# Performance work log

Hardware: AMD Instinct MI355X
Metric: run time of the kernel (lower is better)

The kernel has to match this reference:

```python
import jax, jax.numpy as jnp
import numpy as np

B, N, T, W, H, ED, S, C, E = 16, 256, 64, 12, 64, 64, 5, 4, 2048
ALPHA = 1.0
FG = W + H  # gcn_in_channels = window_size + tgcn_hidden_dim


def setup_inputs() -> dict:
    key = jax.random.key(0)
    ks = jax.random.split(key, 26)
    rn = lambda k, shape: jax.random.normal(k, shape, jnp.float32) * 0.1
    x = jax.random.normal(ks[0], (B, N, T), jnp.float32)
    src = jax.random.randint(ks[1], (E,), 0, N)
    off = jax.random.randint(ks[2], (E,), 1, N)
    dst = (src + off) % N  # no self loops
    return {
        'x': x,
        'static_edge_weight': jax.random.uniform(ks[3], (E,), jnp.float32),
        'gsl_gconv_w': rn(ks[4], (FG, ED)), 'gsl_gconv_b': rn(ks[5], (ED,)),
        'gsl_w1': rn(ks[6], (ED, ED)), 'gsl_b1': rn(ks[7], (ED,)),
        'gsl_w2': rn(ks[8], (ED, ED)), 'gsl_b2': rn(ks[9], (ED,)),
        'wz_c': rn(ks[10], (1, H)), 'bz_c': rn(ks[11], (H,)),
        'wz_l': rn(ks[12], (2 * H, H)), 'bz_l': rn(ks[13], (H,)),
        'wr_c': rn(ks[14], (1, H)), 'br_c': rn(ks[15], (H,)),
        'wr_l': rn(ks[16], (2 * H, H)), 'br_l': rn(ks[17], (H,)),
        'wh_c': rn(ks[18], (1, H)), 'bh_c': rn(ks[19], (H,)),
        'wh_l': rn(ks[20], (2 * H, H)), 'bh_l': rn(ks[21], (H,)),
        'cls_w': rn(ks[22], (N * H, C)), 'cls_b': rn(ks[23], (C,)),
        'static_edge_index': jnp.stack([src, dst]).astype(jnp.int32),
    }


def _normalize(A):
    # GCN sym-norm with added self loops; A has zero diagonal by construction.
    Ahat = A + jnp.eye(N, dtype=A.dtype)
    deg = Ahat.sum(axis=-2)  # in-degree (PyG gcn_norm scatters weight on col)
    dinv = jnp.where(deg > 0, 1.0 / jnp.sqrt(deg), 0.0)
    return dinv[..., :, None] * Ahat * dinv[..., None, :]


def reference(x, static_edge_weight, gsl_gconv_w, gsl_gconv_b, gsl_w1, gsl_b1,
              gsl_w2, gsl_b2, wz_c, bz_c, wz_l, bz_l, wr_c, br_c, wr_l, br_l,
              wh_c, bh_c, wh_l, bh_l, cls_w, cls_b, static_edge_index):
    A_stat = jnp.zeros((N, N), jnp.float32).at[static_edge_index[0], static_edge_index[1]].add(static_edge_weight)
    An_stat = _normalize(A_stat)  # [N,N]

    # Sliding windows, left-padded with zeros to window_size W.
    xp = jnp.pad(x, ((0, 0), (0, 0), (W - 1, 0)))
    widx = jnp.arange(T)[:, None] + jnp.arange(W)[None, :]
    wins = jnp.transpose(xp[:, :, widx], (2, 0, 1, 3))      # [T,B,N,W]
    xts = jnp.transpose(x, (2, 0, 1))[..., None]            # [T,B,N,1]
    cnts = jnp.minimum(jnp.arange(T) + 1, S).astype(jnp.float32)
    idxs = jnp.arange(T) % S

    def gcn_s(X, Wm, b):  # static graph, out[j] = sum_i Anorm[i,j] (XW)[i]
        return jnp.einsum('ij,bif->bjf', An_stat, X @ Wm) + b

    def gcn_d(An, X, Wm, b):  # per-batch dynamic graph
        return jnp.einsum('bij,bif->bjf', An, X @ Wm) + b

    def step(carry, xs):
        h, Eh = carry
        win, xt, cnt, idx = xs
        It = jnp.concatenate([win, h], axis=-1)             # [B,N,W+H]
        df = gcn_s(It, gsl_gconv_w, gsl_gconv_b)
        de1 = jnp.tanh(ALPHA * (df @ gsl_w1 + gsl_b1))
        de2 = jnp.tanh(ALPHA * (df @ gsl_w2 + gsl_b2))
        M12 = jnp.einsum('bie,bje->bij', de1, de2)          # de1 @ de2^T
        Et = jax.nn.relu(jnp.tanh(ALPHA * (M12 - jnp.swapaxes(M12, -1, -2))))
        Eh = Eh.at[:, idx].set(Et)                          # ring buffer write
        Mt = Eh.sum(axis=1) / cnt                           # mean over filled slots
        An = _normalize(Mt)
        cz = gcn_d(An, xt, wz_c, bz_c)
        z = jax.nn.sigmoid(jnp.concatenate([cz, h], -1) @ wz_l + bz_l)
        cr = gcn_d(An, xt, wr_c, br_c)
        r = jax.nn.sigmoid(jnp.concatenate([cr, h], -1) @ wr_l + br_l)
        ch = gcn_d(An, xt, wh_c, bh_c)
        ht = jnp.tanh(jnp.concatenate([ch, h * r], -1) @ wh_l + bh_l)
        h = z * h + (1.0 - z) * ht
        return (h, Eh), None

    h0 = jnp.zeros((B, N, H), jnp.float32)
    Eh0 = jnp.zeros((B, S, N, N), jnp.float32)
    (hT, _), _ = jax.lax.scan(step, (h0, Eh0), (wins, xts, cnts, idxs))
    return hT.reshape(B, N * H) @ cls_w + cls_b
```

## Files before the change

### kernel.cpp

```cpp
#include <hip/hip_runtime.h>
#include <hip/hip_bf16.h>


typedef unsigned short u16;
typedef unsigned int u32;
typedef __attribute__((ext_vector_type(8))) short bf16x8;
typedef __attribute__((ext_vector_type(4))) float f32x4;

#define B_ 16
#define N_ 256
#define T_ 64
#define W_ 12
#define S_ 5
#define E_ 2048
#define FG_ 76
#define G_ 16

__device__ __forceinline__ float b2f(u16 u) {
  union { u32 i; float f; } v; v.i = ((u32)u) << 16; return v.f;
}
__device__ __forceinline__ u16 f2b(float f) {
  union { float f; u32 i; } v; v.f = f;
  u32 x = v.i; x += 0x7fff + ((x >> 16) & 1); return (u16)(x >> 16);
}
__device__ __forceinline__ float ftanh(float x) {
  float e = __expf(-2.f * fabsf(x));
  float t = (1.f - e) / (1.f + e);
  return x < 0.f ? -t : t;
}
__device__ __forceinline__ float fsigm(float x) { return 1.f / (1.f + __expf(-x)); }
__device__ __forceinline__ float cvload(const void* p, int i, int f) {
  return f ? ((const float*)p)[i] : b2f(((const u16*)p)[i]);
}
__device__ __forceinline__ float gld(const float* p) {
  return __hip_atomic_load(p, __ATOMIC_RELAXED, __HIP_MEMORY_SCOPE_SYSTEM);
}
__device__ __forceinline__ void gst(float* p, float v) {
  __hip_atomic_store(p, v, __ATOMIC_RELAXED, __HIP_MEMORY_SCOPE_SYSTEM);
}
__device__ __forceinline__ u32 gldu(const u32* p) {
  return __hip_atomic_load(p, __ATOMIC_RELAXED, __HIP_MEMORY_SCOPE_SYSTEM);
}
__device__ __forceinline__ void gstu(u32* p, u32 v) {
  __hip_atomic_store(p, v, __ATOMIC_RELAXED, __HIP_MEMORY_SCOPE_SYSTEM);
}
__device__ __forceinline__ f32x4 mfma16(bf16x8 a, bf16x8 b, f32x4 c) {
  return __builtin_amdgcn_mfma_f32_16x16x32_bf16(a, b, c, 0, 0, 0);
}
__device__ __forceinline__ bf16x8 ldfrag(const u16* p) { return *(const bf16x8*)p; }

struct Params {
  const void *x0, *ew0, *gw0, *gb0, *w10, *b10, *w20, *b20;
  const void *wzc0, *bzc0, *wzl0, *bzl0, *wrc0, *brc0, *wrl0, *brl0;
  const void *whc0, *bhc0, *whl0, *bhl0, *clsw0, *clsb0;
  const int* eidx;
  float *xf, *ewf, *gwf, *gbf, *b1f, *b2ff;
  float *wzcf, *bzcf, *wzlf, *bzlf, *wrcf, *brcf, *wrlf, *brlf;
  float *whcf, *bhcf, *whlf, *bhlf, *clswf, *clsbf;
  u16 *w1h, *w2h;
  float *AnT, *dinvS, *uvF, *de1, *de2, *h, *degsum, *Eh, *Ascr;
  u32 *xTp, *hgpT;
  int *bar, *flag;
  void* out;
};

__device__ __forceinline__ void bbar(int* ctr, int& cnt) {
  ++cnt;
  __syncthreads();
  if (threadIdx.x == 0) {
    __hip_atomic_fetch_add(ctr, 1, __ATOMIC_RELAXED, __HIP_MEMORY_SCOPE_SYSTEM);
    const int target = cnt * G_;
    while (__hip_atomic_load(ctr, __ATOMIC_RELAXED, __HIP_MEMORY_SCOPE_SYSTEM) < target)
      __builtin_amdgcn_s_sleep(1);
  }
  __syncthreads();
}

__global__ void k_detect(Params p) {
  if (threadIdx.x == 0) {
    const u16* q = (const u16*)p.x0;
    int c = 0;
    for (int i = 0; i < 256; ++i) {
      int ex = (q[i] >> 7) & 0xff;
      c += (ex >= 110 && ex <= 135);
    }
    *p.flag = (c < 200) ? 1 : 0;
  }
}

__global__ void k_convert(Params p) {
  const int f = *p.flag;
  const int blk = blockIdx.x, tid = threadIdx.x;
  if (blk < 32) {
    const int base = blk * 8192;
    for (int i = tid; i < 8192; i += 256) p.xf[base + i] = cvload(p.x0, base + i, f);
    return;
  }
  if (blk == 51) { for (int i = tid; i < 4096; i += 256) p.w1h[i] = f ? f2b(((const float*)p.w10)[i]) : ((const u16*)p.w10)[i]; return; }
  if (blk == 52) { for (int i = tid; i < 4096; i += 256) p.w2h[i] = f ? f2b(((const float*)p.w20)[i]) : ((const u16*)p.w20)[i]; return; }
  const void* src = nullptr; float* dst = nullptr; int n = 0;
  switch (blk) {
    case 32: src = p.ew0;  dst = p.ewf;  n = E_;      break;
    case 33: src = p.gw0;  dst = p.gwf;  n = FG_ * 64; break;
    case 34: src = p.gb0;  dst = p.gbf;  n = 64;      break;
    case 35: src = p.b10;  dst = p.b1f;  n = 64;      break;
    case 36: src = p.b20;  dst = p.b2ff; n = 64;      break;
    case 37: src = p.wzc0; dst = p.wzcf; n = 64;      break;
    case 38: src = p.bzc0; dst = p.bzcf; n = 64;      break;
    case 39: src = p.wzl0; dst = p.wzlf; n = 8192;    break;
    case 40: src = p.bzl0; dst = p.bzlf; n = 64;      break;
    case 41: src = p.wrc0; dst = p.wrcf; n = 64;      break;
    case 42: src = p.brc0; dst = p.brcf; n = 64;      break;
    case 43: src = p.wrl0; dst = p.wrlf; n = 8192;    break;
    case 44: src = p.brl0; dst = p.brlf; n = 64;      break;
    case 45: src = p.whc0; dst = p.whcf; n = 64;      break;
    case 46: src = p.bhc0; dst = p.bhcf; n = 64;      break;
    case 47: src = p.whl0; dst = p.whlf; n = 8192;    break;
    case 48: src = p.bhl0; dst = p.bhlf; n = 64;      break;
    case 49: src = p.clsw0; dst = p.clswf; n = 65536; break;
    case 50: src = p.clsb0; dst = p.clsbf; n = 4;     break;
    default: return;
  }
  for (int i = tid; i < n; i += 256) dst[i] = cvload(src, i, f);
}

__global__ void k_xt(Params p) {
  __shared__ float tile[64 * 65];
  const int b = blockIdx.x, tid = threadIdx.x;
  for (int chunk = 0; chunk < 4; ++chunk) {
    __syncthreads();
    const int r = tid >> 2, tq = (tid & 3) * 16;
    #pragma unroll
    for (int q = 0; q < 16; ++q)
      tile[r * 65 + tq + q] = p.xf[((size_t)b * N_ + chunk * 64 + r) * T_ + tq + q];
    __syncthreads();
    #pragma unroll
    for (int q = 0; q < 8; ++q) {
      const int idx = q * 256 + tid;
      const int t = idx >> 5, c = idx & 31;
      u32 v = (u32)f2b(tile[(2 * c) * 65 + t]) | ((u32)f2b(tile[(2 * c + 1) * 65 + t]) << 16);
      p.xTp[(size_t)(b * 64 + t) * 128 + chunk * 32 + c] = v;
    }
  }
}

__global__ void k_scatter(Params p) {
  for (int e = threadIdx.x; e < E_; e += 256) {
    int s = p.eidx[e], d = p.eidx[E_ + e];
    atomicAdd(&p.Ascr[s * N_ + d], p.ewf[e]);
  }
}
__global__ void k_deg(Params p) {
  int j = threadIdx.x;
  float dg = 1.f;
  for (int i = 0; i < N_; ++i) dg += p.Ascr[i * N_ + j];
  p.dinvS[j] = rsqrtf(dg);
}
__global__ void k_ant(Params p) {
  int i = blockIdx.x, j = threadIdx.x;
  float a = p.Ascr[i * N_ + j] + (i == j ? 1.f : 0.f);
  p.AnT[j * N_ + i] = p.dinvS[i] * a * p.dinvS[j];
}
__global__ void k_uv(Params p) {
  int e = threadIdx.x; if (e >= 64) return;
  float uz = 0, vz = 0, ur = 0, vr = 0, uh = 0, vh = 0;
  for (int f = 0; f < 64; ++f) {
    float wz = p.wzlf[f * 64 + e], wr = p.wrlf[f * 64 + e], wh = p.whlf[f * 64 + e];
    uz += p.wzcf[f] * wz; vz += p.bzcf[f] * wz;
    ur += p.wrcf[f] * wr; vr += p.brcf[f] * wr;
    uh += p.whcf[f] * wh; vh += p.bhcf[f] * wh;
  }
  p.uvF[0 * 64 + e] = uz; p.uvF[1 * 64 + e] = vz + p.bzlf[e];
  p.uvF[2 * 64 + e] = ur; p.uvF[3 * 64 + e] = vr + p.brlf[e];
  p.uvF[4 * 64 + e] = uh; p.uvF[5 * 64 + e] = vh + p.bhlf[e];
}

__global__ void __launch_bounds__(256) dtgcn_main(Params p) {
  __shared__ __align__(16) u16 s_union[21120];
  __shared__ __align__(16) u16 s_gwF[64 * 104];
  __shared__ __align__(16) u16 s_w1T[64 * 72], s_w2T[64 * 72];
  __shared__ __align__(16) u16 s_gzT[64 * 72], s_grT[64 * 72], s_ghT[64 * 72];
  __shared__ __align__(16) u16 s_antO1[16 * 264], s_antO2[16 * 264];
  __shared__ __align__(16) u16 s_m1[16 * 104];
  __shared__ float s_msum[16 * 257];
  __shared__ __align__(16) u16 s_de1I[16 * 72], s_de2I[16 * 72];
  __shared__ __align__(16) u16 s_hbf[16 * 72];
  __shared__ __align__(16) u16 s_dfhr[16 * 72];
  __shared__ float s_colv[16], s_degacc[16];
  __shared__ float s_y[256], s_dinv[256], s_s[16];
  __shared__ float s_uv[384], s_gb[64], s_b1[64], s_b2[64];

  const int b = blockIdx.x & 15;
  const int wg = blockIdx.x >> 4;
  const int tid = threadIdx.x;
  const int lane = tid & 63;
  const int wv = tid >> 6;
  const int l = lane & 15;
  const int quad = lane >> 4;
  const int r0 = wg * 16;

  for (int idx = tid; idx < 64 * 104; idx += 256) {
    const int ee = idx / 104, k = idx - ee * 104;
    u16 v = 0;
    if (k < 64) v = f2b(p.gwf[(12 + k) * 64 + ee]);
    else if (k < 76) v = f2b(p.gwf[(k - 64) * 64 + ee]);
    s_gwF[ee * 104 + k] = v;
  }
  for (int idx = tid; idx < 4096; idx += 256) {
    const int ee = idx >> 6, ff = idx & 63;
    s_w1T[ee * 72 + ff] = p.w1h[ff * 64 + ee];
    s_w2T[ee * 72 + ff] = p.w2h[ff * 64 + ee];
    s_gzT[ee * 72 + ff] = f2b(p.wzlf[4096 + ff * 64 + ee]);
    s_grT[ee * 72 + ff] = f2b(p.wrlf[4096 + ff * 64 + ee]);
    s_ghT[ee * 72 + ff] = f2b(p.whlf[4096 + ff * 64 + ee]);
    const int j = idx >> 8, i = idx & 255;
    float a = p.AnT[(r0 + j) * N_ + i];
    u16 hi = f2b(a);
    s_antO1[j * 264 + i] = hi;
    s_antO2[j * 264 + i] = f2b(a - b2f(hi));
  }
  for (int idx = tid; idx < 16 * 257; idx += 256) s_msum[idx] = 0.f;
  for (int idx = tid; idx < 16 * 72; idx += 256) s_hbf[idx] = 0;
  for (int idx = tid; idx < 16 * 104; idx += 256) s_m1[idx] = 0;
  for (int idx = tid; idx < 384; idx += 256) s_uv[idx] = p.uvF[idx];
  if (tid < 64) { s_gb[tid] = p.gbf[tid]; s_b1[tid] = p.b1f[tid]; s_b2[tid] = p.b2ff[tid]; }
  if (tid < 16) s_degacc[tid] = 0.f;
  __syncthreads();

  u32*  de1g  = (u32*)p.de1 + (size_t)b * N_ * 32;
  u32*  de2g  = (u32*)p.de2 + (size_t)b * N_ * 32;
  u32*  hgpb  = p.hgpT + (size_t)b * 64 * 128;
  const u32* xTb = p.xTp + (size_t)b * 64 * 128;
  float* hb   = p.h + (size_t)b * N_ * 64;
  float* degb = p.degsum + (size_t)b * N_;
  int* bar = p.bar + b * 64;
  int bcnt = 0;

  u16* s_itT = s_union;
  u16* s_j1  = s_union;
  u16* s_j2  = s_union + 9216;
  float* s_part = (float*)s_union;

  float hreg[4] = {0.f, 0.f, 0.f, 0.f};
  const int e = wv * 16 + l;

  for (int t = 0; t < T_; ++t) {
    {
      u32 th[32], tw[6];
      #pragma unroll
      for (int q = 0; q < 32; ++q) th[q] = gldu(&hgpb[q * 256 + tid]);
      #pragma unroll
      for (int q = 0; q < 6; ++q) {
        const int idx = q * 256 + tid;
        const int w2 = idx >> 7, c = idx & 127;
        const int tx = t - (W_ - 1) + w2;
        tw[q] = (tx >= 0) ? gldu(&xTb[(size_t)tx * 128 + c]) : 0u;
      }
      __syncthreads();
      #pragma unroll
      for (int q = 0; q < 32; ++q) {
        const int idx = q * 256 + tid;
        const int k = idx >> 7, c = idx & 127;
        *(u32*)&s_itT[k * 264 + 2 * c] = th[q];
      }
      #pragma unroll
      for (int q = 0; q < 6; ++q) {
        const int idx = q * 256 + tid;
        const int w2 = idx >> 7, c = idx & 127;
        *(u32*)&s_itT[(64 + w2) * 264 + 2 * c] = tw[q];
      }
      #pragma unroll
      for (int q = 0; q < 2; ++q) {
        const int idx = q * 256 + tid;
        const int k = 76 + (idx >> 7), c = idx & 127;
        *(u32*)&s_itT[k * 264 + 2 * c] = 0u;
      }
      __syncthreads();
      for (int nt = wv; nt < 5; nt += 4) {
        f32x4 acc = {0.f, 0.f, 0.f, 0.f};
        #pragma unroll
        for (int ch = 0; ch < 8; ++ch) {
          const int io = ch * 32 + quad * 8;
          bf16x8 bfr = ldfrag(&s_itT[(nt * 16 + l) * 264 + io]);
          acc = mfma16(ldfrag(&s_antO1[l * 264 + io]), bfr, acc);
          acc = mfma16(ldfrag(&s_antO2[l * 264 + io]), bfr, acc);
        }
        #pragma unroll
        for (int r = 0; r < 4; ++r)
          s_m1[(quad * 4 + r) * 104 + nt * 16 + l] = f2b(acc[r]);
      }
      __syncthreads();
      {
        f32x4 dfa = {0.f, 0.f, 0.f, 0.f};
        #pragma unroll
        for (int ks = 0; ks < 3; ++ks) {
          bf16x8 afr = ldfrag(&s_m1[l * 104 + ks * 32 + quad * 8]);
          dfa = mfma16(afr, ldfrag(&s_gwF[e * 104 + ks * 32 + quad * 8]), dfa);
        }
        #pragma unroll
        for (int r = 0; r < 4; ++r)
          s_dfhr[(quad * 4 + r) * 72 + e] = f2b(dfa[r] + s_gb[e]);
      }
      __syncthreads();
      {
        f32x4 E1, E2;
        #pragma unroll
        for (int r = 0; r < 4; ++r) { E1[r] = s_b1[e]; E2[r] = s_b2[e]; }
        #pragma unroll
        for (int ks = 0; ks < 2; ++ks) {
          bf16x8 afr = ldfrag(&s_dfhr[l * 72 + ks * 32 + quad * 8]);
          E1 = mfma16(afr, ldfrag(&s_w1T[e * 72 + ks * 32 + quad * 8]), E1);
          E2 = mfma16(afr, ldfrag(&s_w2T[e * 72 + ks * 32 + quad * 8]), E2);
        }
        #pragma unroll
        for (int r = 0; r < 4; ++r) {
          s_de1I[(quad * 4 + r) * 72 + e] = f2b(ftanh(E1[r]));
          s_de2I[(quad * 4 + r) * 72 + e] = f2b(ftanh(E2[r]));
        }
      }
      __syncthreads();
      #pragma unroll
      for (int q = 0; q < 2; ++q) {
        const int idx = q * 256 + tid;
        const int row = idx >> 5, cp = idx & 31;
        u32 v1 = (u32)s_de1I[row * 72 + cp * 2] | ((u32)s_de1I[row * 72 + cp * 2 + 1] << 16);
        u32 v2 = (u32)s_de2I[row * 72 + cp * 2] | ((u32)s_de2I[row * 72 + cp * 2 + 1] << 16);
        gstu(&de1g[(size_t)(r0 + row) * 32 + cp], v1);
        gstu(&de2g[(size_t)(r0 + row) * 32 + cp], v2);
      }
    }
    bbar(bar, bcnt);

    {
      const int sidx = t % S_;
      float* Ehc = p.Eh + (size_t)(b * S_ + sidx) * N_ * N_;
      if (tid < 16) s_colv[tid] = 0.f;
      float dcacc = 0.f;
      bf16x8 b1f_[2], b2f_[2];
      #pragma unroll
      for (int ks = 0; ks < 2; ++ks) {
        b1f_[ks] = ldfrag(&s_de1I[l * 72 + ks * 32 + quad * 8]);
        b2f_[ks] = ldfrag(&s_de2I[l * 72 + ks * 32 + quad * 8]);
      }
      for (int jh = 0; jh < 2; ++jh) {
        u32 t1[16], t2[16];
        #pragma unroll
        for (int q = 0; q < 16; ++q) {
          const int idx = q * 256 + tid;
          const int row = idx >> 5, cp = idx & 31;
          t1[q] = gldu(&de1g[(size_t)(jh * 128 + row) * 32 + cp]);
          t2[q] = gldu(&de2g[(size_t)(jh * 128 + row) * 32 + cp]);
        }
        __syncthreads();
        #pragma unroll
        for (int q = 0; q < 16; ++q) {
          const int idx = q * 256 + tid;
          const int row = idx >> 5, cp = idx & 31;
          *(u32*)&s_j1[row * 72 + cp * 2] = t1[q];
          *(u32*)&s_j2[row * 72 + cp * 2] = t2[q];
        }
        __syncthreads();
        #pragma unroll
        for (int mt2 = 0; mt2 < 2; ++mt2) {
          const int mt = wv * 2 + mt2;
          f32x4 D1 = {0.f, 0.f, 0.f, 0.f}, D2 = {0.f, 0.f, 0.f, 0.f};
          #pragma unroll
          for (int ks = 0; ks < 2; ++ks) {
            bf16x8 af1 = ldfrag(&s_j1[(mt * 16 + l) * 72 + ks * 32 + quad * 8]);
            bf16x8 af2 = ldfrag(&s_j2[(mt * 16 + l) * 72 + ks * 32 + quad * 8]);
            D1 = mfma16(af1, b2f_[ks], D1);
            D2 = mfma16(af2, b1f_[ks], D2);
          }
          #pragma unroll
          for (int r = 0; r < 4; ++r) {
            const int i = jh * 128 + mt * 16 + quad * 4 + r;
            float d = ftanh(D1[r] - D2[r]);
            float eN = fmaxf(d, 0.f);
            float old = Ehc[(r0 + l) * N_ + i];
            float dd = eN - old;
            Ehc[(r0 + l) * N_ + i] = eN;
            s_msum[l * 257 + i] += dd;
            dcacc += dd;
          }
        }
      }
      dcacc += __shfl_xor(dcacc, 16);
      dcacc += __shfl_xor(dcacc, 32);
      if (lane < 16) atomicAdd(&s_colv[lane], dcacc);
      __syncthreads();
      if (tid < 16) {
        float nd = s_degacc[tid] + s_colv[tid];
        s_degacc[tid] = nd;
        gst(&degb[r0 + tid], nd);
      }
    }
    bbar(bar, bcnt);

    {
      const float cnt = (float)((t + 1 < S_) ? (t + 1) : S_);
      const float invc = 1.f / cnt;
      {
        float dg = 1.f + gld(&degb[tid]) * invc;
        float di = rsqrtf(dg);
        float xv = p.xf[((size_t)b * N_ + tid) * T_ + t];
        s_dinv[tid] = di;
        s_y[tid] = di * xv;
      }
      __syncthreads();
      {
        const int jl = tid & 15, c = tid >> 4;
        float part = 0.f;
        #pragma unroll
        for (int k = 0; k < 16; ++k)
          part += s_msum[jl * 257 + c * 16 + k] * s_y[c * 16 + k];
        s_part[c * 16 + jl] = part;
      }
      __syncthreads();
      if (tid < 16) {
        float tot = 0.f;
        for (int k = 0; k < 16; ++k) tot += s_part[k * 16 + tid];
        const int j = r0 + tid;
        s_s[tid] = s_dinv[j] * (tot * invc + s_y[j]);
      }
      __syncthreads();
      float sv[4];
      #pragma unroll
      for (int r = 0; r < 4; ++r) sv[r] = s_s[quad * 4 + r];
      f32x4 az;
      #pragma unroll
      for (int r = 0; r < 4; ++r) az[r] = s_uv[0 * 64 + e] * sv[r] + s_uv[1 * 64 + e];
      #pragma unroll
      for (int ks = 0; ks < 2; ++ks) {
        bf16x8 afr = ldfrag(&s_hbf[l * 72 + ks * 32 + quad * 8]);
        az = mfma16(afr, ldfrag(&s_gzT[e * 72 + ks * 32 + quad * 8]), az);
      }
      float zz[4];
      #pragma unroll
      for (int r = 0; r < 4; ++r) zz[r] = fsigm(az[r]);
      f32x4 ar_;
      #pragma unroll
      for (int r = 0; r < 4; ++r) ar_[r] = s_uv[2 * 64 + e] * sv[r] + s_uv[3 * 64 + e];
      #pragma unroll
      for (int ks = 0; ks < 2; ++ks) {
        bf16x8 afr = ldfrag(&s_hbf[l * 72 + ks * 32 + quad * 8]);
        ar_ = mfma16(afr, ldfrag(&s_grT[e * 72 + ks * 32 + quad * 8]), ar_);
      }
      #pragma unroll
      for (int r = 0; r < 4; ++r)
        s_dfhr[(quad * 4 + r) * 72 + e] = f2b(hreg[r] * fsigm(ar_[r]));
      __syncthreads();
      f32x4 ah;
      #pragma unroll
      for (int r = 0; r < 4; ++r) ah[r] = s_uv[4 * 64 + e] * sv[r] + s_uv[5 * 64 + e];
      #pragma unroll
      for (int ks = 0; ks < 2; ++ks) {
        bf16x8 afr = ldfrag(&s_dfhr[l * 72 + ks * 32 + quad * 8]);
        ah = mfma16(afr, ldfrag(&s_ghT[e * 72 + ks * 32 + quad * 8]), ah);
      }
      #pragma unroll
      for (int r = 0; r < 4; ++r) {
        float ht = ftanh(ah[r]);
        hreg[r] = zz[r] * hreg[r] + (1.f - zz[r]) * ht;
      }
      #pragma unroll
      for (int r = 0; r < 4; ++r)
        s_hbf[(quad * 4 + r) * 72 + e] = f2b(hreg[r]);
      if (t == T_ - 1) {
        #pragma unroll
        for (int r = 0; r < 4; ++r)
          hb[(r0 + quad * 4 + r) * 64 + e] = hreg[r];
      }
      __syncthreads();
      #pragma unroll
      for (int q = 0; q < 2; ++q) {
        const int idx = q * 256 + tid;
        const int k = idx >> 3, c = idx & 7;
        u32 v = (u32)s_hbf[(2 * c) * 72 + k] | ((u32)s_hbf[(2 * c + 1) * 72 + k] << 16);
        gstu(&hgpb[(size_t)k * 128 + (r0 >> 1) + c], v);
      }
    }
    bbar(bar, bcnt);
  }
}

__global__ void k_cls(Params p) {
  __shared__ float red[256][4];
  const int b = blockIdx.x, i = threadIdx.x;
  const float* hr = p.h + ((size_t)b * N_ + i) * 64;
  const float* w = p.clswf + (size_t)i * 64 * 4;
  float a0 = 0, a1 = 0, a2 = 0, a3 = 0;
  for (int f = 0; f < 64; ++f) {
    float hv = hr[f];
    a0 += hv * w[f * 4 + 0]; a1 += hv * w[f * 4 + 1];
    a2 += hv * w[f * 4 + 2]; a3 += hv * w[f * 4 + 3];
  }
  red[i][0] = a0; red[i][1] = a1; red[i][2] = a2; red[i][3] = a3;
  __syncthreads();
  for (int st = 128; st > 0; st >>= 1) {
    if (i < st) {
      red[i][0] += red[i + st][0]; red[i][1] += red[i + st][1];
      red[i][2] += red[i + st][2]; red[i][3] += red[i + st][3];
    }
    __syncthreads();
  }
  if (i < 4) {
    float v = red[0][i] + p.clsbf[i];
    if (*p.flag) ((float*)p.out)[b * 4 + i] = v;
    else         ((u16*)p.out)[b * 4 + i] = f2b(v);
  }
}

extern "C" void kernel_launch(void* const* d_in, const int* in_sizes, int n_in,
                              void* d_out, int out_size, void* d_ws, size_t ws_size,
                              hipStream_t stream) {
  float* w = (float*)d_ws;
  size_t o = 0;
  auto alloc = [&](size_t n) { float* r = w + o; o += (n + 63) & ~(size_t)63; return r; };
  float* xf    = alloc(262144);
  float* ewf   = alloc(E_);
  float* gwf   = alloc(FG_ * 64);
  float* gbf   = alloc(64);
  float* b1f   = alloc(64);
  float* b2ff  = alloc(64);
  float* wzcf  = alloc(64); float* bzcf = alloc(64); float* wzlf = alloc(8192); float* bzlf = alloc(64);
  float* wrcf  = alloc(64); float* brcf = alloc(64); float* wrlf = alloc(8192); float* brlf = alloc(64);
  float* whcf  = alloc(64); float* bhcf = alloc(64); float* whlf = alloc(8192); float* bhlf = alloc(64);
  float* clswf = alloc(65536); float* clsbf = alloc(64);
  u16* w1h = (u16*)alloc(2048);
  u16* w2h = (u16*)alloc(2048);
  int* flag = (int*)alloc(64);
  float* AnT   = alloc(65536);
  float* dinvS = alloc(256);
  float* uvF   = alloc(384);
  float* de1   = alloc((size_t)B_ * N_ * 32);
  float* de2   = alloc((size_t)B_ * N_ * 32);
  u32*   xTp   = (u32*)alloc((size_t)B_ * 64 * 128);
  const size_t zero_off = o;
  float* Ascr  = alloc((size_t)N_ * N_);
  float* h     = alloc((size_t)B_ * N_ * 64);
  u32*   hgpT  = (u32*)alloc((size_t)B_ * 64 * 128);
  float* degs  = alloc((size_t)B_ * N_);
  int*   bar   = (int*)alloc(B_ * 64);
  float* Eh    = alloc((size_t)B_ * S_ * N_ * N_);
  if (ws_size < o * sizeof(float)) return;

  (void)hipMemsetAsync(w + zero_off, 0, (o - zero_off) * sizeof(float), stream);

  Params p;
  p.x0  = d_in[0];  p.ew0 = d_in[1];
  p.gw0 = d_in[2];  p.gb0 = d_in[3];
  p.w10 = d_in[4];  p.b10 = d_in[5];
  p.w20 = d_in[6];  p.b20 = d_in[7];
  p.wzc0 = d_in[8];  p.bzc0 = d_in[9];  p.wzl0 = d_in[10]; p.bzl0 = d_in[11];
  p.wrc0 = d_in[12]; p.brc0 = d_in[13]; p.wrl0 = d_in[14]; p.brl0 = d_in[15];
  p.whc0 = d_in[16]; p.bhc0 = d_in[17]; p.whl0 = d_in[18]; p.bhl0 = d_in[19];
  p.clsw0 = d_in[20]; p.clsb0 = d_in[21];
  p.eidx = (const int*)d_in[22];
  p.xf = xf; p.ewf = ewf; p.gwf = gwf; p.gbf = gbf; p.b1f = b1f; p.b2ff = b2ff;
  p.wzcf = wzcf; p.bzcf = bzcf; p.wzlf = wzlf; p.bzlf = bzlf;
  p.wrcf = wrcf; p.brcf = brcf; p.wrlf = wrlf; p.brlf = brlf;
  p.whcf = whcf; p.bhcf = bhcf; p.whlf = whlf; p.bhlf = bhlf;
  p.clswf = clswf; p.clsbf = clsbf; p.w1h = w1h; p.w2h = w2h;
  p.AnT = AnT; p.dinvS = dinvS; p.uvF = uvF; p.de1 = de1; p.de2 = de2;
  p.h = h; p.degsum = degs; p.Eh = Eh; p.Ascr = Ascr;
  p.xTp = xTp; p.hgpT = hgpT; p.bar = bar; p.flag = flag; p.out = d_out;

  k_detect<<<1, 64, 0, stream>>>(p);
  k_convert<<<53, 256, 0, stream>>>(p);
  k_xt<<<B_, 256, 0, stream>>>(p);
  k_scatter<<<1, 256, 0, stream>>>(p);
  k_deg<<<1, 256, 0, stream>>>(p);
  k_ant<<<N_, 256, 0, stream>>>(p);
  k_uv<<<1, 64, 0, stream>>>(p);

  void* args[] = { &p };
  hipError_t ce = hipLaunchCooperativeKernel((const void*)dtgcn_main,
                                             dim3(B_ * G_), dim3(256), args, 0, stream);
  if (ce != hipSuccess) {
    (void)hipGetLastError();
    dtgcn_main<<<dim3(B_ * G_), dim3(256), 0, stream>>>(p);
  }

  k_cls<<<B_, 256, 0, stream>>>(p);
}
```

Measured before the change: 938.6 us.

## Replace grid barriers with per-workgroup tag flags and read MFMA operands directly from global

Each shared counter barrier between phases is replaced by per-workgroup monotonic tag words. Every workgroup publishes its progress, and consumers poll all 16 tags with a wave-wide vote. The MFMA B-fragments (hidden state and windows) and the de1/de2 A-fragments are now loaded straight from global memory as 64-bit relaxed atomic loads, instead of being staged through a shared-memory union. Stores become 64-bit packed. This removes a full barrier round-trip per phase and the shared staging copies. In exchange, every wave issues scattered global loads per MFMA step, and the tag-based ordering relies on relaxed atomics for visibility.

```diff
diff --git a/kernel.cpp b/kernel.cpp
--- a/kernel.cpp
+++ b/kernel.cpp
@@ -4,6 +4,7 @@
 
 typedef unsigned short u16;
 typedef unsigned int u32;
+typedef unsigned long long u64;
 typedef __attribute__((ext_vector_type(8))) short bf16x8;
 typedef __attribute__((ext_vector_type(4))) float f32x4;
 
@@ -38,16 +39,25 @@
 __device__ __forceinline__ void gst(float* p, float v) {
   __hip_atomic_store(p, v, __ATOMIC_RELAXED, __HIP_MEMORY_SCOPE_SYSTEM);
 }
+__device__ __forceinline__ u64 gld64(const u64* p) {
+  return __hip_atomic_load(p, __ATOMIC_RELAXED, __HIP_MEMORY_SCOPE_SYSTEM);
+}
+__device__ __forceinline__ void gst64(u64* p, u64 v) {
+  __hip_atomic_store(p, v, __ATOMIC_RELAXED, __HIP_MEMORY_SCOPE_SYSTEM);
+}
 __device__ __forceinline__ u32 gldu(const u32* p) {
   return __hip_atomic_load(p, __ATOMIC_RELAXED, __HIP_MEMORY_SCOPE_SYSTEM);
 }
-__device__ __forceinline__ void gstu(u32* p, u32 v) {
-  __hip_atomic_store(p, v, __ATOMIC_RELAXED, __HIP_MEMORY_SCOPE_SYSTEM);
-}
 __device__ __forceinline__ f32x4 mfma16(bf16x8 a, bf16x8 b, f32x4 c) {
   return __builtin_amdgcn_mfma_f32_16x16x32_bf16(a, b, c, 0, 0, 0);
 }
 __device__ __forceinline__ bf16x8 ldfrag(const u16* p) { return *(const bf16x8*)p; }
+__device__ __forceinline__ bf16x8 ldfrag_g(const u64* row, int off64) {
+  union { u64 q[2]; bf16x8 f; } u;
+  u.q[0] = gld64(row + off64);
+  u.q[1] = gld64(row + off64 + 1);
+  return u.f;
+}
 
 struct Params {
   const void *x0, *ew0, *gw0, *gb0, *w10, *b10, *w20, *b20;
@@ -58,22 +68,21 @@
   float *wzcf, *bzcf, *wzlf, *bzlf, *wrcf, *brcf, *wrlf, *brlf;
   float *whcf, *bhcf, *whlf, *bhlf, *clswf, *clsbf;
   u16 *w1h, *w2h;
-  float *AnT, *dinvS, *uvF, *de1, *de2, *h, *degsum, *Eh, *Ascr;
-  u32 *xTp, *hgpT;
-  int *bar, *flag;
+  float *AnT, *dinvS, *uvF, *h, *degsum, *Eh, *Ascr;
+  u64 *de1g, *de2g, *xTp, *hgpT, *zrow;
+  u32 *tags;
+  int *flag;
   void* out;
 };
 
-__device__ __forceinline__ void bbar(int* ctr, int& cnt) {
-  ++cnt;
-  __syncthreads();
-  if (threadIdx.x == 0) {
-    __hip_atomic_fetch_add(ctr, 1, __ATOMIC_RELAXED, __HIP_MEMORY_SCOPE_SYSTEM);
-    const int target = cnt * G_;
-    while (__hip_atomic_load(ctr, __ATOMIC_RELAXED, __HIP_MEMORY_SCOPE_SYSTEM) < target)
-      __builtin_amdgcn_s_sleep(1);
-  }
-  __syncthreads();
+__device__ __forceinline__ void wtag(const u32* tg, u32 target) {
+  const int k = threadIdx.x & 15;
+  while (!__all((int)(gldu(&tg[k]) >= target)))
+    __builtin_amdgcn_s_sleep(1);
+}
+__device__ __forceinline__ void ptag(u32* tg, int wg, u32 val) {
+  if (threadIdx.x == 0)
+    __hip_atomic_store(&tg[wg], val, __ATOMIC_RELAXED, __HIP_MEMORY_SCOPE_SYSTEM);
 }
 
 __global__ void k_detect(Params p) {
@@ -127,6 +136,7 @@
 __global__ void k_xt(Params p) {
   __shared__ float tile[64 * 65];
   const int b = blockIdx.x, tid = threadIdx.x;
+  u32* xT32 = (u32*)p.xTp;
   for (int chunk = 0; chunk < 4; ++chunk) {
     __syncthreads();
     const int r = tid >> 2, tq = (tid & 3) * 16;
@@ -139,7 +149,7 @@
       const int idx = q * 256 + tid;
       const int t = idx >> 5, c = idx & 31;
       u32 v = (u32)f2b(tile[(2 * c) * 65 + t]) | ((u32)f2b(tile[(2 * c + 1) * 65 + t]) << 16);
-      p.xTp[(size_t)(b * 64 + t) * 128 + chunk * 32 + c] = v;
+      xT32[(size_t)(b * 64 + t) * 128 + chunk * 32 + c] = v;
     }
   }
 }
@@ -176,7 +186,6 @@
 }
 
 __global__ void __launch_bounds__(256) dtgcn_main(Params p) {
-  __shared__ __align__(16) u16 s_union[21120];
   __shared__ __align__(16) u16 s_gwF[64 * 104];
   __shared__ __align__(16) u16 s_w1T[64 * 72], s_w2T[64 * 72];
   __shared__ __align__(16) u16 s_gzT[64 * 72], s_grT[64 * 72], s_ghT[64 * 72];
@@ -186,6 +195,7 @@
   __shared__ __align__(16) u16 s_de1I[16 * 72], s_de2I[16 * 72];
   __shared__ __align__(16) u16 s_hbf[16 * 72];
   __shared__ __align__(16) u16 s_dfhr[16 * 72];
+  __shared__ float s_part[256];
   __shared__ float s_colv[16], s_degacc[16];
   __shared__ float s_y[256], s_dinv[256], s_s[16];
   __shared__ float s_uv[384], s_gb[64], s_b1[64], s_b2[64];
@@ -227,61 +237,36 @@
   if (tid < 16) s_degacc[tid] = 0.f;
   __syncthreads();
 
-  u32*  de1g  = (u32*)p.de1 + (size_t)b * N_ * 32;
-  u32*  de2g  = (u32*)p.de2 + (size_t)b * N_ * 32;
-  u32*  hgpb  = p.hgpT + (size_t)b * 64 * 128;
-  const u32* xTb = p.xTp + (size_t)b * 64 * 128;
+  u64* de1g = p.de1g + (size_t)b * N_ * 16;
+  u64* de2g = p.de2g + (size_t)b * N_ * 16;
+  u64* hgpb = p.hgpT + (size_t)b * 64 * 64;
+  const u64* xTb = p.xTp + (size_t)b * 64 * 64;
+  const u64* zrow = p.zrow;
   float* hb   = p.h + (size_t)b * N_ * 64;
   float* degb = p.degsum + (size_t)b * N_;
-  int* bar = p.bar + b * 64;
-  int bcnt = 0;
-
-  u16* s_itT = s_union;
-  u16* s_j1  = s_union;
-  u16* s_j2  = s_union + 9216;
-  float* s_part = (float*)s_union;
+  u32* tgDe = p.tags + b * 64;
+  u32* tgDg = p.tags + b * 64 + 16;
+  u32* tgH  = p.tags + b * 64 + 32;
 
   float hreg[4] = {0.f, 0.f, 0.f, 0.f};
   const int e = wv * 16 + l;
 
   for (int t = 0; t < T_; ++t) {
+    wtag(tgH, (u32)t);
     {
-      u32 th[32], tw[6];
-      #pragma unroll
-      for (int q = 0; q < 32; ++q) th[q] = gldu(&hgpb[q * 256 + tid]);
-      #pragma unroll
-      for (int q = 0; q < 6; ++q) {
-        const int idx = q * 256 + tid;
-        const int w2 = idx >> 7, c = idx & 127;
-        const int tx = t - (W_ - 1) + w2;
-        tw[q] = (tx >= 0) ? gldu(&xTb[(size_t)tx * 128 + c]) : 0u;
-      }
-      __syncthreads();
-      #pragma unroll
-      for (int q = 0; q < 32; ++q) {
-        const int idx = q * 256 + tid;
-        const int k = idx >> 7, c = idx & 127;
-        *(u32*)&s_itT[k * 264 + 2 * c] = th[q];
-      }
-      #pragma unroll
-      for (int q = 0; q < 6; ++q) {
-        const int idx = q * 256 + tid;
-        const int w2 = idx >> 7, c = idx & 127;
-        *(u32*)&s_itT[(64 + w2) * 264 + 2 * c] = tw[q];
-      }
-      #pragma unroll
-      for (int q = 0; q < 2; ++q) {
-        const int idx = q * 256 + tid;
-        const int k = 76 + (idx >> 7), c = idx & 127;
-        *(u32*)&s_itT[k * 264 + 2 * c] = 0u;
-      }
-      __syncthreads();
       for (int nt = wv; nt < 5; nt += 4) {
+        const int k = nt * 16 + l;
+        const u64* rowp;
+        if (k < 64) rowp = hgpb + (size_t)k * 64;
+        else {
+          const int tx = t - (W_ - 1) + (k - 64);
+          rowp = (k < 76 && tx >= 0) ? (xTb + (size_t)tx * 64) : zrow;
+        }
         f32x4 acc = {0.f, 0.f, 0.f, 0.f};
         #pragma unroll
         for (int ch = 0; ch < 8; ++ch) {
+          bf16x8 bfr = ldfrag_g(rowp, ch * 8 + quad * 2);
           const int io = ch * 32 + quad * 8;
-          bf16x8 bfr = ldfrag(&s_itT[(nt * 16 + l) * 264 + io]);
           acc = mfma16(ldfrag(&s_antO1[l * 264 + io]), bfr, acc);
           acc = mfma16(ldfrag(&s_antO2[l * 264 + io]), bfr, acc);
         }
@@ -319,69 +304,53 @@
         }
       }
       __syncthreads();
-      #pragma unroll
-      for (int q = 0; q < 2; ++q) {
-        const int idx = q * 256 + tid;
-        const int row = idx >> 5, cp = idx & 31;
-        u32 v1 = (u32)s_de1I[row * 72 + cp * 2] | ((u32)s_de1I[row * 72 + cp * 2 + 1] << 16);
-        u32 v2 = (u32)s_de2I[row * 72 + cp * 2] | ((u32)s_de2I[row * 72 + cp * 2 + 1] << 16);
-        gstu(&de1g[(size_t)(r0 + row) * 32 + cp], v1);
-        gstu(&de2g[(size_t)(r0 + row) * 32 + cp], v2);
-      }
+      {
+        const int row = tid >> 4, c = tid & 15;
+        u64 v1 = *(const u64*)&s_de1I[row * 72 + c * 4];
+        u64 v2 = *(const u64*)&s_de2I[row * 72 + c * 4];
+        gst64(&de1g[(size_t)(r0 + row) * 16 + c], v1);
+        gst64(&de2g[(size_t)(r0 + row) * 16 + c], v2);
+      }
+      __syncthreads();
+      ptag(tgDe, wg, (u32)(t + 1));
     }
-    bbar(bar, bcnt);
-
+
+    wtag(tgDe, (u32)(t + 1));
     {
       const int sidx = t % S_;
       float* Ehc = p.Eh + (size_t)(b * S_ + sidx) * N_ * N_;
       if (tid < 16) s_colv[tid] = 0.f;
+      bf16x8 bq1[2], bq2[2];
+      #pragma unroll
+      for (int ks = 0; ks < 2; ++ks) {
+        bq1[ks] = ldfrag(&s_de1I[l * 72 + ks * 32 + quad * 8]);
+        bq2[ks] = ldfrag(&s_de2I[l * 72 + ks * 32 + quad * 8]);
+      }
+      __syncthreads();
       float dcacc = 0.f;
-      bf16x8 b1f_[2], b2f_[2];
-      #pragma unroll
-      for (int ks = 0; ks < 2; ++ks) {
-        b1f_[ks] = ldfrag(&s_de1I[l * 72 + ks * 32 + quad * 8]);
-        b2f_[ks] = ldfrag(&s_de2I[l * 72 + ks * 32 + quad * 8]);
-      }
-      for (int jh = 0; jh < 2; ++jh) {
-        u32 t1[16], t2[16];
-        #pragma unroll
-        for (int q = 0; q < 16; ++q) {
-          const int idx = q * 256 + tid;
-          const int row = idx >> 5, cp = idx & 31;
-          t1[q] = gldu(&de1g[(size_t)(jh * 128 + row) * 32 + cp]);
-          t2[q] = gldu(&de2g[(size_t)(jh * 128 + row) * 32 + cp]);
-        }
-        __syncthreads();
-        #pragma unroll
-        for (int q = 0; q < 16; ++q) {
-          const int idx = q * 256 + tid;
-          const int row = idx >> 5, cp = idx & 31;
-          *(u32*)&s_j1[row * 72 + cp * 2] = t1[q];
-          *(u32*)&s_j2[row * 72 + cp * 2] = t2[q];
-        }
-        __syncthreads();
-        #pragma unroll
-        for (int mt2 = 0; mt2 < 2; ++mt2) {
-          const int mt = wv * 2 + mt2;
-          f32x4 D1 = {0.f, 0.f, 0.f, 0.f}, D2 = {0.f, 0.f, 0.f, 0.f};
-          #pragma unroll
-          for (int ks = 0; ks < 2; ++ks) {
-            bf16x8 af1 = ldfrag(&s_j1[(mt * 16 + l) * 72 + ks * 32 + quad * 8]);
-            bf16x8 af2 = ldfrag(&s_j2[(mt * 16 + l) * 72 + ks * 32 + quad * 8]);
-            D1 = mfma16(af1, b2f_[ks], D1);
-            D2 = mfma16(af2, b1f_[ks], D2);
-          }
-          #pragma unroll
-          for (int r = 0; r < 4; ++r) {
-            const int i = jh * 128 + mt * 16 + quad * 4 + r;
-            float d = ftanh(D1[r] - D2[r]);
-            float eN = fmaxf(d, 0.f);
-            float old = Ehc[(r0 + l) * N_ + i];
-            float dd = eN - old;
-            Ehc[(r0 + l) * N_ + i] = eN;
-            s_msum[l * 257 + i] += dd;
-            dcacc += dd;
-          }
+      #pragma unroll
+      for (int q = 0; q < 4; ++q) {
+        const int mt = wv * 4 + q;
+        const u64* r1 = de1g + (size_t)(mt * 16 + l) * 16;
+        const u64* r2 = de2g + (size_t)(mt * 16 + l) * 16;
+        f32x4 D1 = {0.f, 0.f, 0.f, 0.f}, D2 = {0.f, 0.f, 0.f, 0.f};
+        #pragma unroll
+        for (int ks = 0; ks < 2; ++ks) {
+          bf16x8 a1 = ldfrag_g(r1, ks * 8 + quad * 2);
+          bf16x8 a2 = ldfrag_g(r2, ks * 8 + quad * 2);
+          D1 = mfma16(a1, bq2[ks], D1);
+          D2 = mfma16(a2, bq1[ks], D2);
+        }
+        #pragma unroll
+        for (int r = 0; r < 4; ++r) {
+          const int i = mt * 16 + quad * 4 + r;
+          float d = ftanh(D1[r] - D2[r]);
+          float eN = fmaxf(d, 0.f);
+          float old = Ehc[(r0 + l) * N_ + i];
+          float dd = eN - old;
+          Ehc[(r0 + l) * N_ + i] = eN;
+          s_msum[l * 257 + i] += dd;
+          dcacc += dd;
         }
       }
       dcacc += __shfl_xor(dcacc, 16);
@@ -393,9 +362,11 @@
         s_degacc[tid] = nd;
         gst(&degb[r0 + tid], nd);
       }
+      __syncthreads();
+      ptag(tgDg, wg, (u32)(t + 1));
     }
-    bbar(bar, bcnt);
-
+
+    wtag(tgDg, (u32)(t + 1));
     {
       const float cnt = (float)((t + 1 < S_) ? (t + 1) : S_);
       const float invc = 1.f / cnt;
@@ -471,15 +442,17 @@
           hb[(r0 + quad * 4 + r) * 64 + e] = hreg[r];
       }
       __syncthreads();
-      #pragma unroll
-      for (int q = 0; q < 2; ++q) {
-        const int idx = q * 256 + tid;
-        const int k = idx >> 3, c = idx & 7;
-        u32 v = (u32)s_hbf[(2 * c) * 72 + k] | ((u32)s_hbf[(2 * c + 1) * 72 + k] << 16);
-        gstu(&hgpb[(size_t)k * 128 + (r0 >> 1) + c], v);
-      }
+      {
+        const int k = tid >> 2, c4 = tid & 3;
+        u64 v = (u64)s_hbf[(c4 * 4 + 0) * 72 + k]
+              | ((u64)s_hbf[(c4 * 4 + 1) * 72 + k] << 16)
+              | ((u64)s_hbf[(c4 * 4 + 2) * 72 + k] << 32)
+              | ((u64)s_hbf[(c4 * 4 + 3) * 72 + k] << 48);
+        gst64(&hgpb[(size_t)k * 64 + (r0 >> 2) + c4], v);
+      }
+      __syncthreads();
+      ptag(tgH, wg, (u32)(t + 1));
     }
-    bbar(bar, bcnt);
   }
 }
 
@@ -532,15 +505,16 @@
   float* AnT   = alloc(65536);
   float* dinvS = alloc(256);
   float* uvF   = alloc(384);
-  float* de1   = alloc((size_t)B_ * N_ * 32);
-  float* de2   = alloc((size_t)B_ * N_ * 32);
-  u32*   xTp   = (u32*)alloc((size_t)B_ * 64 * 128);
+  u64* de1g = (u64*)alloc((size_t)B_ * N_ * 32);
+  u64* de2g = (u64*)alloc((size_t)B_ * N_ * 32);
+  u64* xTp  = (u64*)alloc((size_t)B_ * 64 * 128);
   const size_t zero_off = o;
   float* Ascr  = alloc((size_t)N_ * N_);
   float* h     = alloc((size_t)B_ * N_ * 64);
-  u32*   hgpT  = (u32*)alloc((size_t)B_ * 64 * 128);
+  u64*   hgpT  = (u64*)alloc((size_t)B_ * 64 * 128);
   float* degs  = alloc((size_t)B_ * N_);
-  int*   bar   = (int*)alloc(B_ * 64);
+  u64*   zrow  = (u64*)alloc(128);
+  u32*   tags  = (u32*)alloc(B_ * 64);
   float* Eh    = alloc((size_t)B_ * S_ * N_ * N_);
   if (ws_size < o * sizeof(float)) return;
 
@@ -561,9 +535,10 @@
   p.wrcf = wrcf; p.brcf = brcf; p.wrlf = wrlf; p.brlf = brlf;
   p.whcf = whcf; p.bhcf = bhcf; p.whlf = whlf; p.bhlf = bhlf;
   p.clswf = clswf; p.clsbf = clsbf; p.w1h = w1h; p.w2h = w2h;
-  p.AnT = AnT; p.dinvS = dinvS; p.uvF = uvF; p.de1 = de1; p.de2 = de2;
+  p.AnT = AnT; p.dinvS = dinvS; p.uvF = uvF;
   p.h = h; p.degsum = degs; p.Eh = Eh; p.Ascr = Ascr;
-  p.xTp = xTp; p.hgpT = hgpT; p.bar = bar; p.flag = flag; p.out = d_out;
+  p.de1g = de1g; p.de2g = de2g; p.xTp = xTp; p.hgpT = hgpT; p.zrow = zrow;
+  p.tags = tags; p.flag = flag; p.out = d_out;
 
   k_detect<<<1, 64, 0, stream>>>(p);
   k_convert<<<53, 256, 0, stream>>>(p);
```

New measurement: 1.172 ms. 1.25x slower.
